# Performance work log

Hardware: AMD Instinct MI355X
Metric: run time of the kernel (lower is better)

The kernel has to match this reference:

```python
import jax, jax.numpy as jnp
import numpy as np

N0, N1, N2 = 100000, 50000, 8000   # src/dst node counts per block (dst = first n_dst of src)
E0, E1 = 600000, 80000             # edges per block
F_IN, HID, H, C = 256, 64, 4, 47   # in feats, hidden per head, heads, classes
NEG_SLOPE = 0.2


def setup_inputs() -> dict:
    key = jax.random.key(0)
    ks = jax.random.split(key, 12)
    rn = lambda k, shape, s=1.0: jax.random.normal(k, shape, jnp.float32) * s
    return {
        "x":   rn(ks[0], (N0, F_IN)),
        "W1":  rn(ks[1], (F_IN, H * HID), 0.05),
        "al1": rn(ks[2], (H, HID), 0.1),
        "ar1": rn(ks[3], (H, HID), 0.1),
        "b1":  jnp.zeros((H * HID,), jnp.float32),
        "W2":  rn(ks[4], (H * HID, H * C), 0.05),
        "al2": rn(ks[5], (H, C), 0.1),
        "ar2": rn(ks[6], (H, C), 0.1),
        "b2":  jnp.zeros((H * C,), jnp.float32),
        "src0": jax.random.randint(ks[7], (E0,), 0, N0, jnp.int32),
        "dst0": jax.random.randint(ks[8], (E0,), 0, N1, jnp.int32),
        "src1": jax.random.randint(ks[9], (E1,), 0, N1, jnp.int32),
        "dst1": jax.random.randint(ks[10], (E1,), 0, N2, jnp.int32),
    }


def gat_conv(h, src, dst, n_dst, W, attn_l, attn_r, bias):
    """DGL GATConv on a bipartite block: dst nodes = first n_dst src nodes."""
    nh, d = attn_l.shape
    feat = (h @ W).reshape(-1, nh, d)                     # [N_src, H, D]
    el = jnp.einsum('nhd,hd->nh', feat, attn_l)           # [N_src, H]
    er = jnp.einsum('nhd,hd->nh', feat[:n_dst], attn_r)   # [N_dst, H]
    e = jax.nn.leaky_relu(el[src] + er[dst], NEG_SLOPE)   # [E, H]
    # segment (edge) softmax over destination neighborhoods
    m = jax.ops.segment_max(e, dst, num_segments=n_dst)   # [N_dst, H]
    ee = jnp.exp(e - m[dst])
    s = jax.ops.segment_sum(ee, dst, num_segments=n_dst)
    alpha = ee / s[dst]                                   # [E, H]
    # scatter-weighted aggregation of source features
    out = jax.ops.segment_sum(alpha[:, :, None] * feat[src], dst, num_segments=n_dst)
    return out + bias.reshape(1, nh, d)                   # [N_dst, H, D]


def reference(x, W1, al1, ar1, b1, W2, al2, ar2, b2, src0, dst0, src1, dst1):
    h = gat_conv(x, src0, dst0, N1, W1, al1, ar1, b1)     # [N1, H, HID]
    h = jax.nn.elu(h).reshape(N1, -1)                     # activation + flatten heads
    h = gat_conv(h, src1, dst1, N2, W2, al2, ar2, b2)     # [N2, H, C], no activation on last layer
    return h.mean(axis=1)                                 # mean over heads -> [N2, C]
```

## Files before the change

### kernel.cpp

```cpp
#include <hip/hip_runtime.h>

#define CN0 100000
#define CN1 50000
#define CN2 8000
#define CE0 600000
#define CE1 80000
#define CFIN 256
#define CHID 64
#define CNH 4
#define CNC 47
#define CHD1 256
#define CHC2 188

static __host__ __device__ inline int cdiv(int a, int b) { return (a + b - 1) / b; }

typedef __bf16 bf16x8 __attribute__((ext_vector_type(8)));
typedef __bf16 bf16x4 __attribute__((ext_vector_type(4)));
typedef float f32x16 __attribute__((ext_vector_type(16)));

__global__ __launch_bounds__(256) void prep_w_kernel(const float* __restrict__ W,
                                                     __bf16* __restrict__ WTh,
                                                     __bf16* __restrict__ WTl, int N) {
    int id = blockIdx.x * 256 + threadIdx.x;
    if (id >= N * 256) return;
    int n = id >> 8, k = id & 255;
    float w = W[(size_t)k * N + n];
    __bf16 h = (__bf16)w;
    WTh[id] = h;
    WTl[id] = (__bf16)(w - (float)h);
}

#define KP 40
__global__ __launch_bounds__(256) void gemm_mfma_kernel(const float* __restrict__ A,
                                                        const __bf16* __restrict__ BTh,
                                                        const __bf16* __restrict__ BTl,
                                                        float* __restrict__ C,
                                                        int M, int N, int K) {
    __shared__ __align__(16) __bf16 Ah[128 * KP];
    __shared__ __align__(16) __bf16 Al[128 * KP];
    __shared__ __align__(16) __bf16 Bh[128 * KP];
    __shared__ __align__(16) __bf16 Bl[128 * KP];
    int tid = threadIdx.x;
    int wave = tid >> 6, lane = tid & 63;
    int rowBase = blockIdx.x * 128, colBase = blockIdx.y * 128;
    int wr = wave >> 1, wc = wave & 1;

    f32x16 acc[2][2];
#pragma unroll
    for (int m = 0; m < 2; m++)
#pragma unroll
        for (int n = 0; n < 2; n++)
#pragma unroll
            for (int r = 0; r < 16; r++) acc[m][n][r] = 0.f;

    int arow = tid >> 1;
    int akc = (tid & 1) * 16;
    int bcol = tid & 127;
    int bsel = tid >> 7;
    bool avalid = (rowBase + arow) < M;
    const float* aptr = &A[(size_t)(rowBase + arow) * K + akc];
    int gcol = colBase + bcol;
    const __bf16* bptr = (bsel ? BTl : BTh) + (size_t)gcol * K;
    __bf16* bdst = (bsel ? Bl : Bh) + bcol * KP;

    int rc = lane & 31;
    int kb = (lane >> 5) * 8;

    for (int k0 = 0; k0 < K; k0 += 32) {
#pragma unroll
        for (int c = 0; c < 4; c++) {
            float4 v = avalid ? *reinterpret_cast<const float4*>(aptr + k0 + c * 4)
                              : make_float4(0.f, 0.f, 0.f, 0.f);
            __bf16 h0 = (__bf16)v.x, h1 = (__bf16)v.y, h2 = (__bf16)v.z, h3 = (__bf16)v.w;
            bf16x4 hv = {h0, h1, h2, h3};
            bf16x4 lv = {(__bf16)(v.x - (float)h0), (__bf16)(v.y - (float)h1),
                         (__bf16)(v.z - (float)h2), (__bf16)(v.w - (float)h3)};
            int o = arow * KP + akc + c * 4;
            *reinterpret_cast<bf16x4*>(&Ah[o]) = hv;
            *reinterpret_cast<bf16x4*>(&Al[o]) = lv;
        }
        if (gcol < N) {
#pragma unroll
            for (int c = 0; c < 4; c++) {
                bf16x8 v = *reinterpret_cast<const bf16x8*>(&bptr[k0 + c * 8]);
                *reinterpret_cast<bf16x8*>(&bdst[c * 8]) = v;
            }
        } else {
#pragma unroll
            for (int c = 0; c < 4; c++) {
                bf16x8 z = {};
                *reinterpret_cast<bf16x8*>(&bdst[c * 8]) = z;
            }
        }
        __syncthreads();

#pragma unroll
        for (int ks = 0; ks < 32; ks += 16) {
            bf16x8 fah[2], fal[2], fbh[2], fbl[2];
#pragma unroll
            for (int m = 0; m < 2; m++) {
                int r = wr * 64 + m * 32 + rc;
                fah[m] = *reinterpret_cast<const bf16x8*>(&Ah[r * KP + ks + kb]);
                fal[m] = *reinterpret_cast<const bf16x8*>(&Al[r * KP + ks + kb]);
            }
#pragma unroll
            for (int n = 0; n < 2; n++) {
                int cL = wc * 64 + n * 32 + rc;
                fbh[n] = *reinterpret_cast<const bf16x8*>(&Bh[cL * KP + ks + kb]);
                fbl[n] = *reinterpret_cast<const bf16x8*>(&Bl[cL * KP + ks + kb]);
            }
#pragma unroll
            for (int m = 0; m < 2; m++)
#pragma unroll
                for (int n = 0; n < 2; n++) {
                    acc[m][n] = __builtin_amdgcn_mfma_f32_32x32x16_bf16(fah[m], fbh[n],
                                                                        acc[m][n], 0, 0, 0);
                    acc[m][n] = __builtin_amdgcn_mfma_f32_32x32x16_bf16(fah[m], fbl[n],
                                                                        acc[m][n], 0, 0, 0);
                    acc[m][n] = __builtin_amdgcn_mfma_f32_32x32x16_bf16(fal[m], fbh[n],
                                                                        acc[m][n], 0, 0, 0);
                }
        }
        __syncthreads();
    }

#pragma unroll
    for (int m = 0; m < 2; m++)
#pragma unroll
        for (int n = 0; n < 2; n++) {
            int col = colBase + wc * 64 + n * 32 + rc;
            if (col >= N) continue;
            int rbase = rowBase + wr * 64 + m * 32 + 4 * (lane >> 5);
#pragma unroll
            for (int r = 0; r < 16; r++) {
                int row = rbase + (r & 3) + 8 * (r >> 2);
                if (row < M) C[(size_t)row * N + col] = acc[m][n][r];
            }
        }
}

__global__ __launch_bounds__(256) void scores1_kernel(const float* __restrict__ feat,
                                                      const float* __restrict__ al,
                                                      const float* __restrict__ ar,
                                                      float* __restrict__ el,
                                                      float* __restrict__ er, int n_dst) {
    int n = blockIdx.x;
    int tid = threadIdx.x;
    int h = tid >> 6, dd = tid & 63;
    float f = feat[(size_t)n * CHD1 + tid];
    float pl = f * al[h * CHID + dd];
    float pr = f * ar[h * CHID + dd];
#pragma unroll
    for (int off = 32; off > 0; off >>= 1) {
        pl += __shfl_down(pl, off);
        pr += __shfl_down(pr, off);
    }
    if (dd == 0) {
        el[n * CNH + h] = pl;
        if (n < n_dst) er[n * CNH + h] = pr;
    }
}

__global__ __launch_bounds__(192) void scores2_kernel(const float* __restrict__ feat,
                                                      const float* __restrict__ al,
                                                      const float* __restrict__ ar,
                                                      float* __restrict__ el,
                                                      float* __restrict__ er, int n_dst) {
    int n = blockIdx.x;
    int tid = threadIdx.x;
    __shared__ float pl[CHC2], pr[CHC2];
    if (tid < CHC2) {
        float f = feat[(size_t)n * CHC2 + tid];
        pl[tid] = f * al[tid];
        pr[tid] = f * ar[tid];
    }
    __syncthreads();
    if (tid < CNH) {
        float sl = 0.f, sr = 0.f;
        for (int c = 0; c < CNC; c++) {
            sl += pl[tid * CNC + c];
            sr += pr[tid * CNC + c];
        }
        el[n * CNH + tid] = sl;
        if (n < n_dst) er[n * CNH + tid] = sr;
    }
}

__global__ void hist_kernel(const int* __restrict__ dst, int* __restrict__ counts, int E) {
    int i = blockIdx.x * blockDim.x + threadIdx.x;
    if (i < E) atomicAdd(&counts[dst[i]], 1);
}

__global__ __launch_bounds__(256) void scan1_kernel(const int* __restrict__ cnt,
                                                    int* __restrict__ rp,
                                                    int* __restrict__ bsums, int n) {
    __shared__ int sm[256];
    int b = blockIdx.x, tid = threadIdx.x;
    int base = b * 1024 + tid * 4;
    int v0 = 0, v1 = 0, v2 = 0, v3 = 0;
    if (base + 3 < n) {
        int4 q = *reinterpret_cast<const int4*>(&cnt[base]);
        v0 = q.x; v1 = q.y; v2 = q.z; v3 = q.w;
    } else {
        if (base + 0 < n) v0 = cnt[base + 0];
        if (base + 1 < n) v1 = cnt[base + 1];
        if (base + 2 < n) v2 = cnt[base + 2];
        if (base + 3 < n) v3 = cnt[base + 3];
    }
    int s1 = v0 + v1, s2 = s1 + v2, s3 = s2 + v3;
    sm[tid] = s3;
    __syncthreads();
    for (int off = 1; off < 256; off <<= 1) {
        int t = (tid >= off) ? sm[tid - off] : 0;
        __syncthreads();
        sm[tid] += t;
        __syncthreads();
    }
    int prefix = (tid > 0) ? sm[tid - 1] : 0;
    if (base + 0 < n) rp[base + 1] = prefix + v0;
    if (base + 1 < n) rp[base + 2] = prefix + s1;
    if (base + 2 < n) rp[base + 3] = prefix + s2;
    if (base + 3 < n) rp[base + 4] = prefix + s3;
    if (tid == 255) bsums[b] = sm[255];
    if (b == 0 && tid == 0) rp[0] = 0;
}

__global__ __launch_bounds__(256) void scan2_kernel(int* __restrict__ bsums, int nb) {
    __shared__ int sm[256];
    int tid = threadIdx.x;
    int v = (tid < nb) ? bsums[tid] : 0;
    sm[tid] = v;
    __syncthreads();
    for (int off = 1; off < 256; off <<= 1) {
        int t = (tid >= off) ? sm[tid - off] : 0;
        __syncthreads();
        sm[tid] += t;
        __syncthreads();
    }
    if (tid < nb) bsums[tid] = sm[tid] - v;
}

__global__ __launch_bounds__(256) void scan3_kernel(int* __restrict__ rp,
                                                    const int* __restrict__ bsums, int n) {
    int b = blockIdx.x, tid = threadIdx.x;
    if (b == 0) return;
    int add = bsums[b];
    int idx = b * 1024 + tid * 4;
#pragma unroll
    for (int u = 1; u <= 4; u++) {
        int p = idx + u;
        if (p <= n) rp[p] += add;
    }
}

__global__ void scatter_kernel(const int* __restrict__ dst, const int* __restrict__ src,
                               int* __restrict__ cursor, int* __restrict__ csrsrc, int E) {
    int i = blockIdx.x * blockDim.x + threadIdx.x;
    if (i < E) {
        int p = atomicAdd(&cursor[dst[i]], 1);
        csrsrc[p] = src[i];
    }
}

__global__ __launch_bounds__(256) void alpha_kernel(const float* __restrict__ el,
                                                    const float* __restrict__ er,
                                                    const int* __restrict__ rp,
                                                    const int* __restrict__ csrsrc,
                                                    float* __restrict__ alpha, int n_dst) {
    int wid = (blockIdx.x * 256 + threadIdx.x) >> 6;
    int lane = threadIdx.x & 63;
    if (wid >= n_dst) return;
    int begin = rp[wid], end = rp[wid + 1];
    float4 erv = *reinterpret_cast<const float4*>(&er[wid * 4]);
    float m[4], s[4];
#pragma unroll
    for (int h = 0; h < 4; h++) { m[h] = -1e30f; s[h] = 0.f; }
    for (int i = begin + lane; i < end; i += 64) {
        int sn = csrsrc[i];
        float4 elv = *reinterpret_cast<const float4*>(&el[sn * 4]);
        float v[4] = {elv.x + erv.x, elv.y + erv.y, elv.z + erv.z, elv.w + erv.w};
#pragma unroll
        for (int h = 0; h < 4; h++) {
            float vv = v[h] > 0.f ? v[h] : 0.2f * v[h];
            float nm = fmaxf(m[h], vv);
            s[h] = s[h] * __expf(m[h] - nm) + __expf(vv - nm);
            m[h] = nm;
        }
    }
#pragma unroll
    for (int off = 1; off < 64; off <<= 1) {
#pragma unroll
        for (int h = 0; h < 4; h++) {
            float om = __shfl_xor(m[h], off);
            float os = __shfl_xor(s[h], off);
            float nm = fmaxf(m[h], om);
            s[h] = s[h] * __expf(m[h] - nm) + os * __expf(om - nm);
            m[h] = nm;
        }
    }
    float inv[4];
#pragma unroll
    for (int h = 0; h < 4; h++) inv[h] = s[h] > 0.f ? 1.f / s[h] : 0.f;
    for (int i = begin + lane; i < end; i += 64) {
        int sn = csrsrc[i];
        float4 elv = *reinterpret_cast<const float4*>(&el[sn * 4]);
        float v[4] = {elv.x + erv.x, elv.y + erv.y, elv.z + erv.z, elv.w + erv.w};
        float a[4];
#pragma unroll
        for (int h = 0; h < 4; h++) {
            float vv = v[h] > 0.f ? v[h] : 0.2f * v[h];
            a[h] = __expf(vv - m[h]) * inv[h];
        }
        *reinterpret_cast<float4*>(&alpha[(size_t)i * 4]) = make_float4(a[0], a[1], a[2], a[3]);
    }
}

#define CHUNK 128
__global__ __launch_bounds__(256) void agg1_kernel(const float* __restrict__ feat,
                                                   const float* __restrict__ alpha,
                                                   const int* __restrict__ rp,
                                                   const int* __restrict__ csrsrc,
                                                   const float* __restrict__ bias,
                                                   float* __restrict__ h1) {
    int dstn = blockIdx.x;
    int tid = threadIdx.x;
    int wave = tid >> 6, lane = tid & 63;
    __shared__ int s_src[CHUNK];
    __shared__ __align__(16) float s_alpha[CHUNK][4];
    __shared__ __align__(16) float s_red[3][256];
    int begin = rp[dstn], end = rp[dstn + 1];
    int head = lane >> 4;
    float4 acc = make_float4(0.f, 0.f, 0.f, 0.f);

    for (int cbase = begin; cbase < end; cbase += CHUNK) {
        int cn = min(end - cbase, CHUNK);
        for (int j = tid; j < cn; j += 256) {
            s_src[j] = csrsrc[cbase + j];
            *reinterpret_cast<float4*>(&s_alpha[j][0]) =
                *reinterpret_cast<const float4*>(&alpha[(size_t)(cbase + j) * 4]);
        }
        __syncthreads();
        for (int j = wave; j < cn; j += 4) {
            int sn = s_src[j];
            float a = s_alpha[j][head];
            float4 f = *reinterpret_cast<const float4*>(&feat[(size_t)sn * CHD1 + lane * 4]);
            acc.x += a * f.x; acc.y += a * f.y; acc.z += a * f.z; acc.w += a * f.w;
        }
        __syncthreads();
    }
    if (wave > 0) *reinterpret_cast<float4*>(&s_red[wave - 1][lane * 4]) = acc;
    __syncthreads();
    if (wave == 0) {
#pragma unroll
        for (int w = 0; w < 3; w++) {
            float4 o = *reinterpret_cast<float4*>(&s_red[w][lane * 4]);
            acc.x += o.x; acc.y += o.y; acc.z += o.z; acc.w += o.w;
        }
        float4 b = *reinterpret_cast<const float4*>(&bias[lane * 4]);
        float r[4] = {acc.x + b.x, acc.y + b.y, acc.z + b.z, acc.w + b.w};
#pragma unroll
        for (int u = 0; u < 4; u++) r[u] = r[u] > 0.f ? r[u] : expm1f(r[u]);
        *reinterpret_cast<float4*>(&h1[(size_t)dstn * CHD1 + lane * 4]) =
            make_float4(r[0], r[1], r[2], r[3]);
    }
}

__global__ __launch_bounds__(256) void agg2_kernel(const float* __restrict__ feat,
                                                   const float* __restrict__ alpha,
                                                   const int* __restrict__ rp,
                                                   const int* __restrict__ csrsrc,
                                                   const float* __restrict__ bias,
                                                   float* __restrict__ out) {
    int dstn = blockIdx.x;
    int tid = threadIdx.x;
    int wave = tid >> 6, lane = tid & 63;
    __shared__ int s_src[CHUNK];
    __shared__ __align__(16) float s_alpha[CHUNK][4];
    __shared__ float s_red[3][192];
    __shared__ float s_out[192];
    int begin = rp[dstn], end = rp[dstn + 1];
    int f0 = lane, f1 = lane + 64, f2 = lane + 128;
    int h0 = f0 / CNC, h1_ = f1 / CNC, h2 = f2 < CHC2 ? f2 / CNC : 3;
    float a0c = 0.f, a1c = 0.f, a2c = 0.f;

    for (int cbase = begin; cbase < end; cbase += CHUNK) {
        int cn = min(end - cbase, CHUNK);
        for (int j = tid; j < cn; j += 256) {
            s_src[j] = csrsrc[cbase + j];
            *reinterpret_cast<float4*>(&s_alpha[j][0]) =
                *reinterpret_cast<const float4*>(&alpha[(size_t)(cbase + j) * 4]);
        }
        __syncthreads();
        for (int j = wave; j < cn; j += 4) {
            int sn = s_src[j];
            const float* fr = &feat[(size_t)sn * CHC2];
            a0c += s_alpha[j][h0] * fr[f0];
            a1c += s_alpha[j][h1_] * fr[f1];
            if (f2 < CHC2) a2c += s_alpha[j][h2] * fr[f2];
        }
        __syncthreads();
    }
    if (wave > 0) {
        s_red[wave - 1][f0] = a0c;
        s_red[wave - 1][f1] = a1c;
        if (f2 < 192) s_red[wave - 1][f2] = a2c;
    }
    __syncthreads();
    if (wave == 0) {
#pragma unroll
        for (int w = 0; w < 3; w++) {
            a0c += s_red[w][f0];
            a1c += s_red[w][f1];
            if (f2 < 192) a2c += s_red[w][f2];
        }
        s_out[f0] = a0c + bias[f0];
        if (f1 < CHC2) s_out[f1] = a1c + bias[f1];
        if (f2 < CHC2) s_out[f2] = a2c + bias[f2];
    }
    __syncthreads();
    if (tid < CNC) {
        out[(size_t)dstn * CNC + tid] =
            0.25f * (s_out[tid] + s_out[CNC + tid] + s_out[2 * CNC + tid] + s_out[3 * CNC + tid]);
    }
}

extern "C" void kernel_launch(void* const* d_in, const int* in_sizes, int n_in,
                              void* d_out, int out_size, void* d_ws, size_t ws_size,
                              hipStream_t stream) {
    const float* x   = (const float*)d_in[0];
    const float* W1  = (const float*)d_in[1];
    const float* al1 = (const float*)d_in[2];
    const float* ar1 = (const float*)d_in[3];
    const float* b1  = (const float*)d_in[4];
    const float* W2  = (const float*)d_in[5];
    const float* al2 = (const float*)d_in[6];
    const float* ar2 = (const float*)d_in[7];
    const float* b2  = (const float*)d_in[8];
    const int* src0  = (const int*)d_in[9];
    const int* dst0  = (const int*)d_in[10];
    const int* src1  = (const int*)d_in[11];
    const int* dst1  = (const int*)d_in[12];
    float* out = (float*)d_out;

    char* base = (char*)d_ws;
    size_t off = 0;
    auto carve = [&](size_t bytes) {
        void* p = base + off;
        off = (off + bytes + 255) & ~(size_t)255;
        return p;
    };
    float* feat1   = (float*)carve((size_t)CN0 * CHD1 * 4);
    float* h1      = (float*)carve((size_t)CN1 * CHD1 * 4);
    float* el1     = (float*)carve((size_t)CN0 * CNH * 4);
    float* er1     = (float*)carve((size_t)CN1 * CNH * 4);
    int* rp0       = (int*)carve((CN1 + 1) * 4);
    int* cnt0      = (int*)carve(CN1 * 4);
    int* csrsrc0   = (int*)carve((size_t)CE0 * 4);
    float* alpha0  = (float*)carve((size_t)CE0 * CNH * 4);
    int* rp1       = (int*)carve((CN2 + 1) * 4);
    int* cnt1      = (int*)carve(CN2 * 4);
    int* csrsrc1   = (int*)carve((size_t)CE1 * 4);
    float* alpha1  = (float*)carve((size_t)CE1 * CNH * 4);
    int* bsums0    = (int*)carve(64 * 4);
    int* bsums1    = (int*)carve(64 * 4);
    __bf16* W1Th   = (__bf16*)carve((size_t)CHD1 * CFIN * 2);
    __bf16* W1Tl   = (__bf16*)carve((size_t)CHD1 * CFIN * 2);
    __bf16* W2Th   = (__bf16*)carve((size_t)CHC2 * CHD1 * 2);
    __bf16* W2Tl   = (__bf16*)carve((size_t)CHC2 * CHD1 * 2);
    float* feat2 = feat1;
    float* el2 = el1;
    float* er2 = er1;

    prep_w_kernel<<<cdiv(CHD1 * CFIN, 256), 256, 0, stream>>>(W1, W1Th, W1Tl, CHD1);
    prep_w_kernel<<<cdiv(CHC2 * CHD1, 256), 256, 0, stream>>>(W2, W2Th, W2Tl, CHC2);

    hipMemsetAsync(cnt0, 0, CN1 * 4, stream);
    hipMemsetAsync(cnt1, 0, CN2 * 4, stream);
    hist_kernel<<<cdiv(CE0, 256), 256, 0, stream>>>(dst0, cnt0, CE0);
    hist_kernel<<<cdiv(CE1, 256), 256, 0, stream>>>(dst1, cnt1, CE1);
    int nb0 = cdiv(CN1, 1024), nb1 = cdiv(CN2, 1024);
    scan1_kernel<<<nb0, 256, 0, stream>>>(cnt0, rp0, bsums0, CN1);
    scan1_kernel<<<nb1, 256, 0, stream>>>(cnt1, rp1, bsums1, CN2);
    scan2_kernel<<<1, 256, 0, stream>>>(bsums0, nb0);
    scan2_kernel<<<1, 256, 0, stream>>>(bsums1, nb1);
    scan3_kernel<<<nb0, 256, 0, stream>>>(rp0, bsums0, CN1);
    scan3_kernel<<<nb1, 256, 0, stream>>>(rp1, bsums1, CN2);
    hipMemcpyAsync(cnt0, rp0, CN1 * 4, hipMemcpyDeviceToDevice, stream);
    hipMemcpyAsync(cnt1, rp1, CN2 * 4, hipMemcpyDeviceToDevice, stream);
    scatter_kernel<<<cdiv(CE0, 256), 256, 0, stream>>>(dst0, src0, cnt0, csrsrc0, CE0);
    scatter_kernel<<<cdiv(CE1, 256), 256, 0, stream>>>(dst1, src1, cnt1, csrsrc1, CE1);

    gemm_mfma_kernel<<<dim3(cdiv(CN0, 128), cdiv(CHD1, 128)), 256, 0, stream>>>(
        x, W1Th, W1Tl, feat1, CN0, CHD1, CFIN);
    scores1_kernel<<<CN0, 256, 0, stream>>>(feat1, al1, ar1, el1, er1, CN1);
    alpha_kernel<<<cdiv(CN1, 4), 256, 0, stream>>>(el1, er1, rp0, csrsrc0, alpha0, CN1);
    agg1_kernel<<<CN1, 256, 0, stream>>>(feat1, alpha0, rp0, csrsrc0, b1, h1);

    gemm_mfma_kernel<<<dim3(cdiv(CN1, 128), cdiv(CHC2, 128)), 256, 0, stream>>>(
        h1, W2Th, W2Tl, feat2, CN1, CHC2, CHD1);
    scores2_kernel<<<CN1, 192, 0, stream>>>(feat2, al2, ar2, el2, er2, CN2);
    alpha_kernel<<<cdiv(CN2, 4), 256, 0, stream>>>(el2, er2, rp1, csrsrc1, alpha1, CN2);
    agg2_kernel<<<CN2, 256, 0, stream>>>(feat2, alpha1, rp1, csrsrc1, b2, out);
}
```

Measured before the change: 571.4 us.

## Merge CSR build launches, prefetch GEMM tiles, emit pre-split bf16 hidden features

Merges the per-layer weight prep, histogram, scan and scatter kernels into single launches that handle both graph blocks. The scan now writes the scatter cursor directly, which removes the device-to-device copies. The GEMM loads the next K tile into registers while computing the current one. Layer-1 aggregation now writes hi/lo bf16 halves, so the second GEMM reads bf16 input and skips the float split. This cuts launch count and some memory traffic, at the cost of extra register pressure in the GEMM.

```diff
diff --git a/kernel.cpp b/kernel.cpp
--- a/kernel.cpp
+++ b/kernel.cpp
@@ -18,20 +18,36 @@
 typedef __bf16 bf16x4 __attribute__((ext_vector_type(4)));
 typedef float f32x16 __attribute__((ext_vector_type(16)));
 
-__global__ __launch_bounds__(256) void prep_w_kernel(const float* __restrict__ W,
-                                                     __bf16* __restrict__ WTh,
-                                                     __bf16* __restrict__ WTl, int N) {
+__global__ __launch_bounds__(256) void prep_w2_kernel(const float* __restrict__ W1,
+                                                      __bf16* __restrict__ W1Th,
+                                                      __bf16* __restrict__ W1Tl,
+                                                      const float* __restrict__ W2,
+                                                      __bf16* __restrict__ W2Th,
+                                                      __bf16* __restrict__ W2Tl) {
     int id = blockIdx.x * 256 + threadIdx.x;
-    if (id >= N * 256) return;
-    int n = id >> 8, k = id & 255;
-    float w = W[(size_t)k * N + n];
-    __bf16 h = (__bf16)w;
-    WTh[id] = h;
-    WTl[id] = (__bf16)(w - (float)h);
+    const int tot1 = CHD1 * CFIN;
+    if (id < tot1) {
+        int n = id >> 8, k = id & 255;
+        float w = W1[(size_t)k * CHD1 + n];
+        __bf16 h = (__bf16)w;
+        W1Th[id] = h;
+        W1Tl[id] = (__bf16)(w - (float)h);
+    } else {
+        int id2 = id - tot1;
+        if (id2 >= CHC2 * CHD1) return;
+        int n = id2 >> 8, k = id2 & 255;
+        float w = W2[(size_t)k * CHC2 + n];
+        __bf16 h = (__bf16)w;
+        W2Th[id2] = h;
+        W2Tl[id2] = (__bf16)(w - (float)h);
+    }
 }
 
 #define KP 40
-__global__ __launch_bounds__(256) void gemm_mfma_kernel(const float* __restrict__ A,
+template <bool ASPLIT>
+__global__ __launch_bounds__(256) void gemm_mfma_kernel(const float* __restrict__ Af,
+                                                        const __bf16* __restrict__ Ahp,
+                                                        const __bf16* __restrict__ Alp,
                                                         const __bf16* __restrict__ BTh,
                                                         const __bf16* __restrict__ BTl,
                                                         float* __restrict__ C,
@@ -53,46 +69,76 @@
 #pragma unroll
             for (int r = 0; r < 16; r++) acc[m][n][r] = 0.f;
 
-    int arow = tid >> 1;
-    int akc = (tid & 1) * 16;
-    int bcol = tid & 127;
-    int bsel = tid >> 7;
-    bool avalid = (rowBase + arow) < M;
-    const float* aptr = &A[(size_t)(rowBase + arow) * K + akc];
-    int gcol = colBase + bcol;
+    const int arow = tid >> 1;
+    const int akc = (tid & 1) * 16;
+    const int bcol = tid & 127;
+    const int bsel = tid >> 7;
+    const bool avalid = (rowBase + arow) < M;
+    const int gcol = colBase + bcol;
+    const bool bvalid = gcol < N;
+    const float* aF = &Af[(size_t)(rowBase + arow) * K + akc];
+    const __bf16* aH = &Ahp[(size_t)(rowBase + arow) * K + akc];
+    const __bf16* aL = &Alp[(size_t)(rowBase + arow) * K + akc];
     const __bf16* bptr = (bsel ? BTl : BTh) + (size_t)gcol * K;
     __bf16* bdst = (bsel ? Bl : Bh) + bcol * KP;
 
-    int rc = lane & 31;
-    int kb = (lane >> 5) * 8;
-
-    for (int k0 = 0; k0 < K; k0 += 32) {
-#pragma unroll
-        for (int c = 0; c < 4; c++) {
-            float4 v = avalid ? *reinterpret_cast<const float4*>(aptr + k0 + c * 4)
-                              : make_float4(0.f, 0.f, 0.f, 0.f);
-            __bf16 h0 = (__bf16)v.x, h1 = (__bf16)v.y, h2 = (__bf16)v.z, h3 = (__bf16)v.w;
-            bf16x4 hv = {h0, h1, h2, h3};
-            bf16x4 lv = {(__bf16)(v.x - (float)h0), (__bf16)(v.y - (float)h1),
-                         (__bf16)(v.z - (float)h2), (__bf16)(v.w - (float)h3)};
-            int o = arow * KP + akc + c * 4;
-            *reinterpret_cast<bf16x4*>(&Ah[o]) = hv;
-            *reinterpret_cast<bf16x4*>(&Al[o]) = lv;
-        }
-        if (gcol < N) {
+    const int rc = lane & 31;
+    const int kb = (lane >> 5) * 8;
+
+    float4 pa[4];
+    bf16x8 pah[2], pal[2];
+    bf16x8 pb[4];
+
+    auto LOAD = [&](int k0) {
+        if constexpr (ASPLIT) {
+#pragma unroll
+            for (int c = 0; c < 4; c++)
+                pa[c] = avalid ? *reinterpret_cast<const float4*>(aF + k0 + c * 4)
+                               : make_float4(0.f, 0.f, 0.f, 0.f);
+        } else {
+            bf16x8 z = {};
+            pah[0] = avalid ? *reinterpret_cast<const bf16x8*>(aH + k0) : z;
+            pah[1] = avalid ? *reinterpret_cast<const bf16x8*>(aH + k0 + 8) : z;
+            pal[0] = avalid ? *reinterpret_cast<const bf16x8*>(aL + k0) : z;
+            pal[1] = avalid ? *reinterpret_cast<const bf16x8*>(aL + k0 + 8) : z;
+        }
+        bf16x8 z = {};
+#pragma unroll
+        for (int c = 0; c < 4; c++)
+            pb[c] = bvalid ? *reinterpret_cast<const bf16x8*>(&bptr[k0 + c * 8]) : z;
+    };
+
+    auto STORE = [&]() {
+        if constexpr (ASPLIT) {
 #pragma unroll
             for (int c = 0; c < 4; c++) {
-                bf16x8 v = *reinterpret_cast<const bf16x8*>(&bptr[k0 + c * 8]);
-                *reinterpret_cast<bf16x8*>(&bdst[c * 8]) = v;
+                float4 v = pa[c];
+                __bf16 h0 = (__bf16)v.x, h1 = (__bf16)v.y, h2 = (__bf16)v.z, h3 = (__bf16)v.w;
+                bf16x4 hv = {h0, h1, h2, h3};
+                bf16x4 lv = {(__bf16)(v.x - (float)h0), (__bf16)(v.y - (float)h1),
+                             (__bf16)(v.z - (float)h2), (__bf16)(v.w - (float)h3)};
+                int o = arow * KP + akc + c * 4;
+                *reinterpret_cast<bf16x4*>(&Ah[o]) = hv;
+                *reinterpret_cast<bf16x4*>(&Al[o]) = lv;
             }
         } else {
-#pragma unroll
-            for (int c = 0; c < 4; c++) {
-                bf16x8 z = {};
-                *reinterpret_cast<bf16x8*>(&bdst[c * 8]) = z;
-            }
-        }
-        __syncthreads();
+            int o = arow * KP + akc;
+            *reinterpret_cast<bf16x8*>(&Ah[o]) = pah[0];
+            *reinterpret_cast<bf16x8*>(&Ah[o + 8]) = pah[1];
+            *reinterpret_cast<bf16x8*>(&Al[o]) = pal[0];
+            *reinterpret_cast<bf16x8*>(&Al[o + 8]) = pal[1];
+        }
+#pragma unroll
+        for (int c = 0; c < 4; c++) *reinterpret_cast<bf16x8*>(&bdst[c * 8]) = pb[c];
+    };
+
+    const int nK = K >> 5;
+    LOAD(0);
+    for (int t = 0; t < nK; t++) {
+        __syncthreads();
+        STORE();
+        __syncthreads();
+        if (t + 1 < nK) LOAD((t + 1) * 32);
 
 #pragma unroll
         for (int ks = 0; ks < 32; ks += 16) {
@@ -121,7 +167,6 @@
                                                                         acc[m][n], 0, 0, 0);
                 }
         }
-        __syncthreads();
     }
 
 #pragma unroll
@@ -186,16 +231,28 @@
     }
 }
 
-__global__ void hist_kernel(const int* __restrict__ dst, int* __restrict__ counts, int E) {
+__global__ void hist2_kernel(const int* __restrict__ dst0, int* __restrict__ cnt0,
+                             const int* __restrict__ dst1, int* __restrict__ cnt1) {
     int i = blockIdx.x * blockDim.x + threadIdx.x;
-    if (i < E) atomicAdd(&counts[dst[i]], 1);
-}
-
-__global__ __launch_bounds__(256) void scan1_kernel(const int* __restrict__ cnt,
-                                                    int* __restrict__ rp,
-                                                    int* __restrict__ bsums, int n) {
+    if (i < CE0) {
+        atomicAdd(&cnt0[dst0[i]], 1);
+    } else {
+        int j = i - CE0;
+        if (j < CE1) atomicAdd(&cnt1[dst1[j]], 1);
+    }
+}
+
+__global__ __launch_bounds__(256) void scan1_kernel(const int* __restrict__ cnt0,
+                                                    int* __restrict__ rp0, int* __restrict__ cur0,
+                                                    int* __restrict__ bsums0, int nb0,
+                                                    const int* __restrict__ cnt1,
+                                                    int* __restrict__ rp1, int* __restrict__ cur1,
+                                                    int* __restrict__ bsums1) {
     __shared__ int sm[256];
-    int b = blockIdx.x, tid = threadIdx.x;
+    int gb = blockIdx.x, tid = threadIdx.x;
+    const int* cnt; int* rp; int* cur; int* bsums; int n; int b;
+    if (gb < nb0) { cnt = cnt0; rp = rp0; cur = cur0; bsums = bsums0; n = CN1; b = gb; }
+    else          { cnt = cnt1; rp = rp1; cur = cur1; bsums = bsums1; n = CN2; b = gb - nb0; }
     int base = b * 1024 + tid * 4;
     int v0 = 0, v1 = 0, v2 = 0, v3 = 0;
     if (base + 3 < n) {
@@ -217,17 +274,20 @@
         __syncthreads();
     }
     int prefix = (tid > 0) ? sm[tid - 1] : 0;
-    if (base + 0 < n) rp[base + 1] = prefix + v0;
-    if (base + 1 < n) rp[base + 2] = prefix + s1;
-    if (base + 2 < n) rp[base + 3] = prefix + s2;
-    if (base + 3 < n) rp[base + 4] = prefix + s3;
+    if (base + 0 < n) { rp[base + 1] = prefix + v0; cur[base + 0] = prefix; }
+    if (base + 1 < n) { rp[base + 2] = prefix + s1; cur[base + 1] = prefix + v0; }
+    if (base + 2 < n) { rp[base + 3] = prefix + s2; cur[base + 2] = prefix + s1; }
+    if (base + 3 < n) { rp[base + 4] = prefix + s3; cur[base + 3] = prefix + s2; }
     if (tid == 255) bsums[b] = sm[255];
     if (b == 0 && tid == 0) rp[0] = 0;
 }
 
-__global__ __launch_bounds__(256) void scan2_kernel(int* __restrict__ bsums, int nb) {
+__global__ __launch_bounds__(256) void scan2_kernel(int* __restrict__ bsums0, int nb0,
+                                                    int* __restrict__ bsums1, int nb1) {
     __shared__ int sm[256];
     int tid = threadIdx.x;
+    int* bsums = (blockIdx.x == 0) ? bsums0 : bsums1;
+    int nb = (blockIdx.x == 0) ? nb0 : nb1;
     int v = (tid < nb) ? bsums[tid] : 0;
     sm[tid] = v;
     __syncthreads();
@@ -240,25 +300,39 @@
     if (tid < nb) bsums[tid] = sm[tid] - v;
 }
 
-__global__ __launch_bounds__(256) void scan3_kernel(int* __restrict__ rp,
-                                                    const int* __restrict__ bsums, int n) {
-    int b = blockIdx.x, tid = threadIdx.x;
+__global__ __launch_bounds__(256) void scan3_kernel(int* __restrict__ rp0, int* __restrict__ cur0,
+                                                    const int* __restrict__ bsums0, int nb0,
+                                                    int* __restrict__ rp1, int* __restrict__ cur1,
+                                                    const int* __restrict__ bsums1) {
+    int gb = blockIdx.x, tid = threadIdx.x;
+    int* rp; int* cur; const int* bsums; int n; int b;
+    if (gb < nb0) { rp = rp0; cur = cur0; bsums = bsums0; n = CN1; b = gb; }
+    else          { rp = rp1; cur = cur1; bsums = bsums1; n = CN2; b = gb - nb0; }
     if (b == 0) return;
     int add = bsums[b];
     int idx = b * 1024 + tid * 4;
 #pragma unroll
-    for (int u = 1; u <= 4; u++) {
+    for (int u = 0; u < 4; u++) {
         int p = idx + u;
-        if (p <= n) rp[p] += add;
-    }
-}
-
-__global__ void scatter_kernel(const int* __restrict__ dst, const int* __restrict__ src,
-                               int* __restrict__ cursor, int* __restrict__ csrsrc, int E) {
+        if (p < n) cur[p] += add;
+        if (p + 1 <= n) rp[p + 1] += add;
+    }
+}
+
+__global__ void scatter2_kernel(const int* __restrict__ dst0, const int* __restrict__ src0,
+                                int* __restrict__ cur0, int* __restrict__ csr0,
+                                const int* __restrict__ dst1, const int* __restrict__ src1,
+                                int* __restrict__ cur1, int* __restrict__ csr1) {
     int i = blockIdx.x * blockDim.x + threadIdx.x;
-    if (i < E) {
-        int p = atomicAdd(&cursor[dst[i]], 1);
-        csrsrc[p] = src[i];
+    if (i < CE0) {
+        int p = atomicAdd(&cur0[dst0[i]], 1);
+        csr0[p] = src0[i];
+    } else {
+        int j = i - CE0;
+        if (j < CE1) {
+            int p = atomicAdd(&cur1[dst1[j]], 1);
+            csr1[p] = src1[j];
+        }
     }
 }
 
@@ -321,7 +395,8 @@
                                                    const int* __restrict__ rp,
                                                    const int* __restrict__ csrsrc,
                                                    const float* __restrict__ bias,
-                                                   float* __restrict__ h1) {
+                                                   __bf16* __restrict__ h1h,
+                                                   __bf16* __restrict__ h1l) {
     int dstn = blockIdx.x;
     int tid = threadIdx.x;
     int wave = tid >> 6, lane = tid & 63;
@@ -358,10 +433,16 @@
         }
         float4 b = *reinterpret_cast<const float4*>(&bias[lane * 4]);
         float r[4] = {acc.x + b.x, acc.y + b.y, acc.z + b.z, acc.w + b.w};
-#pragma unroll
-        for (int u = 0; u < 4; u++) r[u] = r[u] > 0.f ? r[u] : expm1f(r[u]);
-        *reinterpret_cast<float4*>(&h1[(size_t)dstn * CHD1 + lane * 4]) =
-            make_float4(r[0], r[1], r[2], r[3]);
+        bf16x4 hv, lv;
+#pragma unroll
+        for (int u = 0; u < 4; u++) {
+            float e = r[u] > 0.f ? r[u] : expm1f(r[u]);
+            __bf16 h = (__bf16)e;
+            hv[u] = h;
+            lv[u] = (__bf16)(e - (float)h);
+        }
+        *reinterpret_cast<bf16x4*>(&h1h[(size_t)dstn * CHD1 + lane * 4]) = hv;
+        *reinterpret_cast<bf16x4*>(&h1l[(size_t)dstn * CHD1 + lane * 4]) = lv;
     }
 }
 
@@ -450,15 +531,16 @@
         return p;
     };
     float* feat1   = (float*)carve((size_t)CN0 * CHD1 * 4);
-    float* h1      = (float*)carve((size_t)CN1 * CHD1 * 4);
+    __bf16* h1h    = (__bf16*)carve((size_t)CN1 * CHD1 * 2);
+    __bf16* h1l    = (__bf16*)carve((size_t)CN1 * CHD1 * 2);
     float* el1     = (float*)carve((size_t)CN0 * CNH * 4);
     float* er1     = (float*)carve((size_t)CN1 * CNH * 4);
     int* rp0       = (int*)carve((CN1 + 1) * 4);
     int* cnt0      = (int*)carve(CN1 * 4);
+    int* cnt1      = (int*)carve(CN2 * 4);
     int* csrsrc0   = (int*)carve((size_t)CE0 * 4);
     float* alpha0  = (float*)carve((size_t)CE0 * CNH * 4);
     int* rp1       = (int*)carve((CN2 + 1) * 4);
-    int* cnt1      = (int*)carve(CN2 * 4);
     int* csrsrc1   = (int*)carve((size_t)CE1 * 4);
     float* alpha1  = (float*)carve((size_t)CE1 * CNH * 4);
     int* bsums0    = (int*)carve(64 * 4);
@@ -471,33 +553,27 @@
     float* el2 = el1;
     float* er2 = er1;
 
-    prep_w_kernel<<<cdiv(CHD1 * CFIN, 256), 256, 0, stream>>>(W1, W1Th, W1Tl, CHD1);
-    prep_w_kernel<<<cdiv(CHC2 * CHD1, 256), 256, 0, stream>>>(W2, W2Th, W2Tl, CHC2);
-
-    hipMemsetAsync(cnt0, 0, CN1 * 4, stream);
-    hipMemsetAsync(cnt1, 0, CN2 * 4, stream);
-    hist_kernel<<<cdiv(CE0, 256), 256, 0, stream>>>(dst0, cnt0, CE0);
-    hist_kernel<<<cdiv(CE1, 256), 256, 0, stream>>>(dst1, cnt1, CE1);
+    prep_w2_kernel<<<cdiv(CHD1 * CFIN + CHC2 * CHD1, 256), 256, 0, stream>>>(
+        W1, W1Th, W1Tl, W2, W2Th, W2Tl);
+
+    hipMemsetAsync(cnt0, 0, (size_t)(CN1 + CN2 + 64) * 4, stream);
+    hist2_kernel<<<cdiv(CE0 + CE1, 256), 256, 0, stream>>>(dst0, cnt0, dst1, cnt1);
     int nb0 = cdiv(CN1, 1024), nb1 = cdiv(CN2, 1024);
-    scan1_kernel<<<nb0, 256, 0, stream>>>(cnt0, rp0, bsums0, CN1);
-    scan1_kernel<<<nb1, 256, 0, stream>>>(cnt1, rp1, bsums1, CN2);
-    scan2_kernel<<<1, 256, 0, stream>>>(bsums0, nb0);
-    scan2_kernel<<<1, 256, 0, stream>>>(bsums1, nb1);
-    scan3_kernel<<<nb0, 256, 0, stream>>>(rp0, bsums0, CN1);
-    scan3_kernel<<<nb1, 256, 0, stream>>>(rp1, bsums1, CN2);
-    hipMemcpyAsync(cnt0, rp0, CN1 * 4, hipMemcpyDeviceToDevice, stream);
-    hipMemcpyAsync(cnt1, rp1, CN2 * 4, hipMemcpyDeviceToDevice, stream);
-    scatter_kernel<<<cdiv(CE0, 256), 256, 0, stream>>>(dst0, src0, cnt0, csrsrc0, CE0);
-    scatter_kernel<<<cdiv(CE1, 256), 256, 0, stream>>>(dst1, src1, cnt1, csrsrc1, CE1);
-
-    gemm_mfma_kernel<<<dim3(cdiv(CN0, 128), cdiv(CHD1, 128)), 256, 0, stream>>>(
-        x, W1Th, W1Tl, feat1, CN0, CHD1, CFIN);
+    scan1_kernel<<<nb0 + nb1, 256, 0, stream>>>(cnt0, rp0, cnt0, bsums0, nb0,
+                                                cnt1, rp1, cnt1, bsums1);
+    scan2_kernel<<<2, 256, 0, stream>>>(bsums0, nb0, bsums1, nb1);
+    scan3_kernel<<<nb0 + nb1, 256, 0, stream>>>(rp0, cnt0, bsums0, nb0, rp1, cnt1, bsums1);
+    scatter2_kernel<<<cdiv(CE0 + CE1, 256), 256, 0, stream>>>(dst0, src0, cnt0, csrsrc0,
+                                                              dst1, src1, cnt1, csrsrc1);
+
+    gemm_mfma_kernel<true><<<dim3(cdiv(CN0, 128), cdiv(CHD1, 128)), 256, 0, stream>>>(
+        x, nullptr, nullptr, W1Th, W1Tl, feat1, CN0, CHD1, CFIN);
     scores1_kernel<<<CN0, 256, 0, stream>>>(feat1, al1, ar1, el1, er1, CN1);
     alpha_kernel<<<cdiv(CN1, 4), 256, 0, stream>>>(el1, er1, rp0, csrsrc0, alpha0, CN1);
-    agg1_kernel<<<CN1, 256, 0, stream>>>(feat1, alpha0, rp0, csrsrc0, b1, h1);
-
-    gemm_mfma_kernel<<<dim3(cdiv(CN1, 128), cdiv(CHC2, 128)), 256, 0, stream>>>(
-        h1, W2Th, W2Tl, feat2, CN1, CHC2, CHD1);
+    agg1_kernel<<<CN1, 256, 0, stream>>>(feat1, alpha0, rp0, csrsrc0, b1, h1h, h1l);
+
+    gemm_mfma_kernel<false><<<dim3(cdiv(CN1, 128), cdiv(CHC2, 128)), 256, 0, stream>>>(
+        nullptr, h1h, h1l, W2Th, W2Tl, feat2, CN1, CHC2, CHD1);
     scores2_kernel<<<CN1, 192, 0, stream>>>(feat2, al2, ar2, el2, er2, CN2);
     alpha_kernel<<<cdiv(CN2, 4), 256, 0, stream>>>(el2, er2, rp1, csrsrc1, alpha1, CN2);
     agg2_kernel<<<CN2, 256, 0, stream>>>(feat2, alpha1, rp1, csrsrc1, b2, out);
```

New measurement: 552.1 us. 1.03x faster.
